# Kernel optimization log

Measured on AMD Instinct MI355X. Metric: run time of the kernel, lower is better.

Reference implementation:

```python
import jax, jax.numpy as jnp
import numpy as np

B, D_FEAT, D_ATTR, N_CLS = 512, 2048, 312, 150


def setup_inputs() -> dict:
    key = jax.random.key(0)
    k1, k2, k3, k4, k5 = jax.random.split(key, 5)
    return {
        "x_f": jax.random.normal(k1, (B, D_FEAT), dtype=jnp.float32),
        "W": jax.random.normal(k2, (D_FEAT, D_ATTR), dtype=jnp.float32) * 0.02,
        "b": jax.random.normal(k3, (D_ATTR,), dtype=jnp.float32) * 0.02,
        "seen_att": jax.random.normal(k4, (N_CLS, D_ATTR), dtype=jnp.float32),
        "x_labels": jax.random.randint(k5, (B,), 0, N_CLS, dtype=jnp.int64),
    }


def reference(x_f, W, b, seen_att, x_labels):
    temp = 1.0
    pre_attr = x_f @ W + b                                # [B, D]
    log_p = jax.nn.log_softmax(pre_attr / temp, axis=-1)  # log pre_attr_softmax
    log_g = jax.nn.log_softmax(seen_att[x_labels] / temp, axis=-1)
    g = jnp.exp(log_g)                                    # gt_attr_softmax [B, D]

    # pairwise KL(target = g_i/g_j || input_logits = log(p_i/p_j)), reduction='sum':
    #   sum_d t * (log t - log_ratio_p)
    t_ratio = g[:, None, :] / g[None, :, :]                               # [B, B, D]
    log_t = log_g[:, None, :] - log_g[None, :, :]                         # [B, B, D]
    log_r = log_p[:, None, :] - log_p[None, :, :]                         # [B, B, D]
    kl = jnp.sum(t_ratio * (log_t - log_r), axis=-1)                      # [B, B]

    same = x_labels[:, None] == x_labels[None, :]
    upper = jnp.triu(jnp.ones((x_labels.shape[0],) * 2, dtype=bool), k=1)
    mask = same & upper

    count = jnp.sum(mask)
    loss = jnp.sum(jnp.where(mask, kl, 0.0))
    return jnp.where(count > 0, loss / count.astype(loss.dtype), loss)
```

## Files before the change

### kernel.cpp

```cpp
#include <hip/hip_runtime.h>
#include <math.h>

#define B      512
#define DF     2048
#define DA     312
#define NTHR   320
#define RT     8
#define KSPLIT 16
#define NRG    (B / RT)

__device__ __forceinline__ float wave_max_f(float v) {
  #pragma unroll
  for (int off = 32; off >= 1; off >>= 1)
    v = fmaxf(v, __shfl_down(v, off));
  return v;
}

__device__ __forceinline__ double wave_sum_d(double v) {
  #pragma unroll
  for (int off = 32; off >= 1; off >>= 1)
    v += __shfl_down(v, off);
  return v;
}

template <int KC>
__global__ __launch_bounds__(NTHR, 5) void gemm_partial_kernel(
    const float* __restrict__ x_f, const float* __restrict__ W,
    float* __restrict__ part) {
  const int c    = threadIdx.x;
  const int rg   = blockIdx.x;
  const int ks   = blockIdx.y;
  const int row0 = rg * RT;
  const int k0   = ks * KC;
  const int ksplit = DF / KC;

  if (c >= DA) return;

  float acc[RT];
  #pragma unroll
  for (int r = 0; r < RT; ++r) acc[r] = 0.f;

  const float* Wp = W + (size_t)k0 * DA + c;
  const float* xp = x_f + (size_t)row0 * DF + k0;

  float wc[8];
  #pragma unroll
  for (int j = 0; j < 8; ++j) wc[j] = Wp[(size_t)j * DA];

  #pragma unroll
  for (int k = 0; k < KC; k += 8) {
    float wn[8];
    if (k + 8 < KC) {
      #pragma unroll
      for (int j = 0; j < 8; ++j) wn[j] = Wp[(size_t)(k + 8 + j) * DA];
    }
    #pragma unroll
    for (int r = 0; r < RT; ++r) {
      const float* xr = xp + (size_t)r * DF + k;
      #pragma unroll
      for (int j = 0; j < 8; ++j) acc[r] = fmaf(xr[j], wc[j], acc[r]);
    }
    if (k + 8 < KC) {
      #pragma unroll
      for (int j = 0; j < 8; ++j) wc[j] = wn[j];
    }
  }

  float* pp = part + ((size_t)(rg * ksplit + ks) * RT) * DA + c;
  #pragma unroll
  for (int r = 0; r < RT; ++r) pp[(size_t)r * DA] = acc[r];
}

template <int KS>
__global__ __launch_bounds__(NTHR) void row_stats_kernel(
    const float* __restrict__ part, const float* __restrict__ b,
    double* __restrict__ S) {
  __shared__ float  red_f[8];
  __shared__ double red_d[16];
  __shared__ float  bcast_max;

  const int tid  = threadIdx.x;
  const int wid  = tid >> 6;
  const int lane = tid & 63;
  const int row  = blockIdx.x;
  const int rg   = row / RT;
  const int r    = row & (RT - 1);

  float v = -INFINITY;
  if (tid < DA) {
    const float* pb = part + ((size_t)(rg * KS) * RT + r) * DA + tid;
    float ps[KS];
    #pragma unroll
    for (int p = 0; p < KS; ++p) ps[p] = pb[(size_t)p * RT * DA];
    float s = b[tid];
    #pragma unroll
    for (int p = 0; p < KS; ++p) s += ps[p];
    v = s;
  }

  float m = wave_max_f(v);
  if (lane == 0) red_f[wid] = m;
  __syncthreads();
  if (tid == 0) {
    float mm = red_f[0];
    #pragma unroll
    for (int w = 1; w < NTHR / 64; ++w) mm = fmaxf(mm, red_f[w]);
    bcast_max = mm;
  }
  __syncthreads();
  const float rowmax = bcast_max;

  double e  = (tid < DA) ? exp((double)v - (double)rowmax) : 0.0;
  double sp = (tid < DA) ? (double)v : 0.0;
  double es = wave_sum_d(e);
  double ss = wave_sum_d(sp);
  if (lane == 0) { red_d[wid] = es; red_d[8 + wid] = ss; }
  __syncthreads();
  if (tid == 0) {
    double esum = 0.0, ssum = 0.0;
    #pragma unroll
    for (int w = 0; w < NTHR / 64; ++w) { esum += red_d[w]; ssum += red_d[8 + w]; }
    S[row] = ssum - (double)DA * ((double)rowmax + log(esum));
  }
}

__global__ __launch_bounds__(1024) void pair_reduce_kernel(
    const double* __restrict__ S, const int* __restrict__ labels,
    float* __restrict__ out) {
  __shared__ double    Ss[B];
  __shared__ int       Ls[B];
  __shared__ double    red_d[16];
  __shared__ long long red_i[16];

  const int tid = threadIdx.x;
  if (tid < B) { Ss[tid] = S[tid]; Ls[tid] = labels[tid]; }
  __syncthreads();

  double lsum = 0.0;
  long long lcnt = 0;
  for (int p = tid; p < B * B; p += 1024) {
    int i = p >> 9;
    int j = p & (B - 1);
    if (j > i && Ls[i] == Ls[j]) { lsum += Ss[j] - Ss[i]; lcnt++; }
  }

  #pragma unroll
  for (int off = 32; off >= 1; off >>= 1) {
    lsum += __shfl_down(lsum, off);
    lcnt += __shfl_down(lcnt, off);
  }
  const int wid = tid >> 6, lane = tid & 63;
  if (lane == 0) { red_d[wid] = lsum; red_i[wid] = lcnt; }
  __syncthreads();
  if (tid == 0) {
    double s = 0.0; long long c = 0;
    #pragma unroll
    for (int w = 0; w < 16; ++w) { s += red_d[w]; c += red_i[w]; }
    out[0] = (float)((c > 0) ? s / (double)c : s);
  }
}

extern "C" void kernel_launch(void* const* d_in, const int* in_sizes, int n_in,
                              void* d_out, int out_size, void* d_ws, size_t ws_size,
                              hipStream_t stream) {
  const float* x_f    = (const float*)d_in[0];
  const float* W      = (const float*)d_in[1];
  const float* b      = (const float*)d_in[2];
  const int*   labels = (const int*)d_in[4];

  double* S    = (double*)d_ws;
  float*  part = (float*)((char*)d_ws + 4096);

  if (ws_size >= 4096 + (size_t)KSPLIT * B * DA * 4) {
    dim3 g1(NRG, KSPLIT);
    gemm_partial_kernel<DF / KSPLIT><<<g1, NTHR, 0, stream>>>(x_f, W, part);
    row_stats_kernel<KSPLIT><<<B, NTHR, 0, stream>>>(part, b, S);
  } else {
    dim3 g1(NRG, 2);
    gemm_partial_kernel<DF / 2><<<g1, NTHR, 0, stream>>>(x_f, W, part);
    row_stats_kernel<2><<<B, NTHR, 0, stream>>>(part, b, S);
  }
  pair_reduce_kernel<<<1, 1024, 0, stream>>>(S, labels, (float*)d_out);
}
```

Measured before the change: 112.7 us.

## Fuse split-K GEMM, row stats and pair reduction into one kernel with tickets

Replaces the three separate launches with a single kernel. The last split-K block to finish for each row group, found through an atomic ticket counter, reduces that group's partials and computes the row log-softmax sums. The last row group to finish then performs the pairwise masked reduction. This removes two kernel launches and their gaps, but adds a memset, atomic exchange stores, atomic loads that read through to the last-level cache, and a serial tail in which one 320-thread block does the B×B pair loop instead of a 1024-thread block.

```diff
diff --git a/kernel.cpp b/kernel.cpp
--- a/kernel.cpp
+++ b/kernel.cpp
@@ -8,6 +8,7 @@
 #define RT     8
 #define KSPLIT 16
 #define NRG    (B / RT)
+#define KC     (DF / KSPLIT)
 
 __device__ __forceinline__ float wave_max_f(float v) {
   #pragma unroll
@@ -23,49 +24,189 @@
   return v;
 }
 
-template <int KC>
-__global__ __launch_bounds__(NTHR, 5) void gemm_partial_kernel(
+__device__ __forceinline__ float llc_load_f(const float* p) {
+  return __int_as_float(atomicOr((int*)p, 0));
+}
+__device__ __forceinline__ double llc_load_d(const double* p) {
+  return __longlong_as_double(
+      (long long)atomicOr((unsigned long long*)p, 0ull));
+}
+
+__global__ __launch_bounds__(NTHR) void fused_kernel(
     const float* __restrict__ x_f, const float* __restrict__ W,
-    float* __restrict__ part) {
+    const float* __restrict__ b, const int* __restrict__ labels,
+    float* part, double* S, int* counters, float* out) {
   const int c    = threadIdx.x;
   const int rg   = blockIdx.x;
   const int ks   = blockIdx.y;
   const int row0 = rg * RT;
   const int k0   = ks * KC;
-  const int ksplit = DF / KC;
-
+
+  __shared__ int       ticket_sh;
+  __shared__ float     red_f[8];
+  __shared__ float     bcast_max;
+  __shared__ double    red_d[16];
+  __shared__ long long red_i[8];
+  __shared__ double    Ss[B];
+  __shared__ int       Ls[B];
+
+  if (c < DA) {
+    float acc[RT];
+    #pragma unroll
+    for (int r = 0; r < RT; ++r) acc[r] = 0.f;
+
+    const float* Wp = W + (size_t)k0 * DA + c;
+    const float* xp = x_f + (size_t)row0 * DF + k0;
+
+    float wc[8];
+    #pragma unroll
+    for (int j = 0; j < 8; ++j) wc[j] = Wp[(size_t)j * DA];
+
+    #pragma unroll
+    for (int k = 0; k < KC; k += 8) {
+      float wn[8];
+      if (k + 8 < KC) {
+        #pragma unroll
+        for (int j = 0; j < 8; ++j) wn[j] = Wp[(size_t)(k + 8 + j) * DA];
+      }
+      #pragma unroll
+      for (int r = 0; r < RT; ++r) {
+        const float* xr = xp + (size_t)r * DF + k;
+        #pragma unroll
+        for (int j = 0; j < 8; ++j) acc[r] = fmaf(xr[j], wc[j], acc[r]);
+      }
+      if (k + 8 < KC) {
+        #pragma unroll
+        for (int j = 0; j < 8; ++j) wc[j] = wn[j];
+      }
+    }
+
+    float* pp = part + ((size_t)(rg * KSPLIT + ks) * RT) * DA + c;
+    float sink = 0.f;
+    #pragma unroll
+    for (int r = 0; r < RT; ++r)
+      sink += atomicExch(&pp[(size_t)r * DA], acc[r]);
+    asm volatile("" :: "v"(sink));
+  }
+
+  asm volatile("s_waitcnt vmcnt(0)" ::: "memory");
+  __syncthreads();
+  if (threadIdx.x == 0)
+    ticket_sh = atomicAdd(&counters[rg], 1);
+  __syncthreads();
+  if (ticket_sh != KSPLIT - 1) return;
+
+  const int wid  = threadIdx.x >> 6;
+  const int lane = threadIdx.x & 63;
+
+  float s[RT];
+  if (c < DA) {
+    const float bias = b[c];
+    #pragma unroll
+    for (int r = 0; r < RT; ++r) {
+      float ps[KSPLIT];
+      #pragma unroll
+      for (int p = 0; p < KSPLIT; ++p)
+        ps[p] = llc_load_f(part + ((size_t)(rg * KSPLIT + p) * RT + r) * DA + c);
+      float acc2 = bias;
+      #pragma unroll
+      for (int p = 0; p < KSPLIT; ++p) acc2 += ps[p];
+      s[r] = acc2;
+    }
+  }
+
+  double ssink = 0.0;
+  for (int r = 0; r < RT; ++r) {
+    float v = (c < DA) ? s[r] : -INFINITY;
+    float m = wave_max_f(v);
+    if (lane == 0) red_f[wid] = m;
+    __syncthreads();
+    if (threadIdx.x == 0) {
+      float mm = red_f[0];
+      #pragma unroll
+      for (int w = 1; w < NTHR / 64; ++w) mm = fmaxf(mm, red_f[w]);
+      bcast_max = mm;
+    }
+    __syncthreads();
+    const float rowmax = bcast_max;
+
+    double e  = (c < DA) ? exp((double)v - (double)rowmax) : 0.0;
+    double sp = (c < DA) ? (double)v : 0.0;
+    double es = wave_sum_d(e);
+    double ss = wave_sum_d(sp);
+    if (lane == 0) { red_d[wid] = es; red_d[8 + wid] = ss; }
+    __syncthreads();
+    if (threadIdx.x == 0) {
+      double esum = 0.0, ssum = 0.0;
+      #pragma unroll
+      for (int w = 0; w < NTHR / 64; ++w) { esum += red_d[w]; ssum += red_d[8 + w]; }
+      double Sval = ssum - (double)DA * ((double)rowmax + log(esum));
+      ssink += __longlong_as_double((long long)atomicExch(
+          (unsigned long long*)&S[row0 + r],
+          (unsigned long long)__double_as_longlong(Sval)));
+    }
+    __syncthreads();
+  }
+  asm volatile("" :: "v"(ssink));
+
+  asm volatile("s_waitcnt vmcnt(0)" ::: "memory");
+  __syncthreads();
+  if (threadIdx.x == 0)
+    ticket_sh = atomicAdd(&counters[NRG], 1);
+  __syncthreads();
+  if (ticket_sh != NRG - 1) return;
+
+  for (int i = threadIdx.x; i < B; i += NTHR) {
+    Ss[i] = llc_load_d(&S[i]);
+    Ls[i] = labels[i];
+  }
+  __syncthreads();
+
+  double lsum = 0.0;
+  long long lcnt = 0;
+  for (int p = threadIdx.x; p < B * B; p += NTHR) {
+    int i = p >> 9;
+    int j = p & (B - 1);
+    if (j > i && Ls[i] == Ls[j]) { lsum += Ss[j] - Ss[i]; lcnt++; }
+  }
+  #pragma unroll
+  for (int off = 32; off >= 1; off >>= 1) {
+    lsum += __shfl_down(lsum, off);
+    lcnt += __shfl_down(lcnt, off);
+  }
+  if (lane == 0) { red_d[wid] = lsum; red_i[wid] = lcnt; }
+  __syncthreads();
+  if (threadIdx.x == 0) {
+    double s2 = 0.0; long long c2 = 0;
+    #pragma unroll
+    for (int w = 0; w < NTHR / 64; ++w) { s2 += red_d[w]; c2 += red_i[w]; }
+    out[0] = (float)((c2 > 0) ? s2 / (double)c2 : s2);
+  }
+}
+
+template <int KCF>
+__global__ __launch_bounds__(NTHR) void gemm_partial_kernel(
+    const float* __restrict__ x_f, const float* __restrict__ W,
+    float* __restrict__ part) {
+  const int c = threadIdx.x, rg = blockIdx.x, ks = blockIdx.y;
+  const int row0 = rg * RT, k0 = ks * KCF, ksplit = DF / KCF;
   if (c >= DA) return;
-
   float acc[RT];
   #pragma unroll
   for (int r = 0; r < RT; ++r) acc[r] = 0.f;
-
   const float* Wp = W + (size_t)k0 * DA + c;
   const float* xp = x_f + (size_t)row0 * DF + k0;
-
-  float wc[8];
-  #pragma unroll
-  for (int j = 0; j < 8; ++j) wc[j] = Wp[(size_t)j * DA];
-
-  #pragma unroll
-  for (int k = 0; k < KC; k += 8) {
-    float wn[8];
-    if (k + 8 < KC) {
-      #pragma unroll
-      for (int j = 0; j < 8; ++j) wn[j] = Wp[(size_t)(k + 8 + j) * DA];
-    }
+  for (int k = 0; k < KCF; k += 8) {
+    float w[8];
+    #pragma unroll
+    for (int j = 0; j < 8; ++j) w[j] = Wp[(size_t)(k + j) * DA];
     #pragma unroll
     for (int r = 0; r < RT; ++r) {
       const float* xr = xp + (size_t)r * DF + k;
       #pragma unroll
-      for (int j = 0; j < 8; ++j) acc[r] = fmaf(xr[j], wc[j], acc[r]);
-    }
-    if (k + 8 < KC) {
-      #pragma unroll
-      for (int j = 0; j < 8; ++j) wc[j] = wn[j];
-    }
-  }
-
+      for (int j = 0; j < 8; ++j) acc[r] = fmaf(xr[j], w[j], acc[r]);
+    }
+  }
   float* pp = part + ((size_t)(rg * ksplit + ks) * RT) * DA + c;
   #pragma unroll
   for (int r = 0; r < RT; ++r) pp[(size_t)r * DA] = acc[r];
@@ -78,26 +219,19 @@
   __shared__ float  red_f[8];
   __shared__ double red_d[16];
   __shared__ float  bcast_max;
-
-  const int tid  = threadIdx.x;
-  const int wid  = tid >> 6;
-  const int lane = tid & 63;
-  const int row  = blockIdx.x;
-  const int rg   = row / RT;
-  const int r    = row & (RT - 1);
-
+  const int tid = threadIdx.x, wid = tid >> 6, lane = tid & 63;
+  const int row = blockIdx.x, rg = row / RT, r = row & (RT - 1);
   float v = -INFINITY;
   if (tid < DA) {
     const float* pb = part + ((size_t)(rg * KS) * RT + r) * DA + tid;
     float ps[KS];
     #pragma unroll
     for (int p = 0; p < KS; ++p) ps[p] = pb[(size_t)p * RT * DA];
-    float s = b[tid];
-    #pragma unroll
-    for (int p = 0; p < KS; ++p) s += ps[p];
-    v = s;
-  }
-
+    float sv = b[tid];
+    #pragma unroll
+    for (int p = 0; p < KS; ++p) sv += ps[p];
+    v = sv;
+  }
   float m = wave_max_f(v);
   if (lane == 0) red_f[wid] = m;
   __syncthreads();
@@ -109,7 +243,6 @@
   }
   __syncthreads();
   const float rowmax = bcast_max;
-
   double e  = (tid < DA) ? exp((double)v - (double)rowmax) : 0.0;
   double sp = (tid < DA) ? (double)v : 0.0;
   double es = wave_sum_d(e);
@@ -131,19 +264,15 @@
   __shared__ int       Ls[B];
   __shared__ double    red_d[16];
   __shared__ long long red_i[16];
-
   const int tid = threadIdx.x;
   if (tid < B) { Ss[tid] = S[tid]; Ls[tid] = labels[tid]; }
   __syncthreads();
-
   double lsum = 0.0;
   long long lcnt = 0;
   for (int p = tid; p < B * B; p += 1024) {
-    int i = p >> 9;
-    int j = p & (B - 1);
+    int i = p >> 9, j = p & (B - 1);
     if (j > i && Ls[i] == Ls[j]) { lsum += Ss[j] - Ss[i]; lcnt++; }
   }
-
   #pragma unroll
   for (int off = 32; off >= 1; off >>= 1) {
     lsum += __shfl_down(lsum, off);
@@ -168,17 +297,21 @@
   const float* b      = (const float*)d_in[2];
   const int*   labels = (const int*)d_in[4];
 
-  double* S    = (double*)d_ws;
-  float*  part = (float*)((char*)d_ws + 4096);
-
-  if (ws_size >= 4096 + (size_t)KSPLIT * B * DA * 4) {
-    dim3 g1(NRG, KSPLIT);
-    gemm_partial_kernel<DF / KSPLIT><<<g1, NTHR, 0, stream>>>(x_f, W, part);
-    row_stats_kernel<KSPLIT><<<B, NTHR, 0, stream>>>(part, b, S);
+  const size_t need = 8192 + (size_t)KSPLIT * B * DA * 4;
+  if (ws_size >= need) {
+    int*    counters = (int*)d_ws;
+    double* S        = (double*)((char*)d_ws + 512);
+    float*  part     = (float*)((char*)d_ws + 8192);
+    hipMemsetAsync(d_ws, 0, 512, stream);
+    dim3 g(NRG, KSPLIT);
+    fused_kernel<<<g, NTHR, 0, stream>>>(x_f, W, b, labels, part, S, counters,
+                                         (float*)d_out);
   } else {
+    double* S    = (double*)d_ws;
+    float*  part = (float*)((char*)d_ws + 4096);
     dim3 g1(NRG, 2);
     gemm_partial_kernel<DF / 2><<<g1, NTHR, 0, stream>>>(x_f, W, part);
     row_stats_kernel<2><<<B, NTHR, 0, stream>>>(part, b, S);
-  }
-  pair_reduce_kernel<<<1, 1024, 0, stream>>>(S, labels, (float*)d_out);
-}
+    pair_reduce_kernel<<<1, 1024, 0, stream>>>(S, labels, (float*)d_out);
+  }
+}
```

Measured after the change: 196.0 us. +73.9%, slower.

## Fuse pair reduction into row-stats kernel via rank-weighted sum and last-block ticket

Applied to the files above, without the earlier changes.

Removes the separate single-block pair_reduce kernel, which scanned all B*B pairs serially on one workgroup. Each row block now computes its label rank and same-label count. It writes coef*S_i and its rank to global memory. A ticket atomic lets the last block finish the reduction, turning the O(B^2) pair loop into an O(B) weighted sum. The cost is an extra label scan per block, atomic/fence ordering that relies on relaxed atomics plus s_waitcnt, and one fewer kernel launch.

```diff
diff --git a/kernel.cpp b/kernel.cpp
--- a/kernel.cpp
+++ b/kernel.cpp
@@ -23,10 +23,23 @@
   return v;
 }
 
+__device__ __forceinline__ void dev_store_d(double* p, double v) {
+  __hip_atomic_store(p, v, __ATOMIC_RELAXED, __HIP_MEMORY_SCOPE_AGENT);
+}
+__device__ __forceinline__ double dev_load_d(const double* p) {
+  return __hip_atomic_load(p, __ATOMIC_RELAXED, __HIP_MEMORY_SCOPE_AGENT);
+}
+__device__ __forceinline__ void dev_store_i(int* p, int v) {
+  __hip_atomic_store(p, v, __ATOMIC_RELAXED, __HIP_MEMORY_SCOPE_AGENT);
+}
+__device__ __forceinline__ int dev_load_i(const int* p) {
+  return __hip_atomic_load(p, __ATOMIC_RELAXED, __HIP_MEMORY_SCOPE_AGENT);
+}
+
 template <int KC>
 __global__ __launch_bounds__(NTHR, 5) void gemm_partial_kernel(
     const float* __restrict__ x_f, const float* __restrict__ W,
-    float* __restrict__ part) {
+    float* __restrict__ part, int* ticket) {
   const int c    = threadIdx.x;
   const int rg   = blockIdx.x;
   const int ks   = blockIdx.y;
@@ -34,6 +47,9 @@
   const int k0   = ks * KC;
   const int ksplit = DF / KC;
 
+  if (blockIdx.x == 0 && blockIdx.y == 0 && threadIdx.x == 0)
+    *ticket = 0;
+
   if (c >= DA) return;
 
   float acc[RT];
@@ -72,12 +88,16 @@
 }
 
 template <int KS>
-__global__ __launch_bounds__(NTHR) void row_stats_kernel(
+__global__ __launch_bounds__(NTHR) void rowstats_pair_kernel(
     const float* __restrict__ part, const float* __restrict__ b,
-    double* __restrict__ S) {
+    const int* __restrict__ labels,
+    double* T, int* RK, int* ticket, float* __restrict__ out) {
   __shared__ float  red_f[8];
   __shared__ double red_d[16];
+  __shared__ int    red_i[16];
   __shared__ float  bcast_max;
+  __shared__ int    ticket_sh;
+  __shared__ int    Lsh[B];
 
   const int tid  = threadIdx.x;
   const int wid  = tid >> 6;
@@ -86,18 +106,150 @@
   const int rg   = row / RT;
   const int r    = row & (RT - 1);
 
+  for (int i = tid; i < B; i += NTHR) Lsh[i] = labels[i];
+
+  float v = -INFINITY;
+  float ps[KS];
+  const bool active = (tid < DA);
+  if (active) {
+    const float* pb = part + ((size_t)(rg * KS) * RT + r) * DA + tid;
+    #pragma unroll
+    for (int p = 0; p < KS; ++p) ps[p] = pb[(size_t)p * RT * DA];
+  }
+
+  __syncthreads();
+
+  const int myl = Lsh[row];
+  int c_less = 0, c_all = 0;
+  for (int j = tid; j < B; j += NTHR) {
+    const int same = (Lsh[j] == myl) ? 1 : 0;
+    c_all += same;
+    if (j < row) c_less += same;
+  }
+  #pragma unroll
+  for (int off = 32; off >= 1; off >>= 1) {
+    c_less += __shfl_down(c_less, off);
+    c_all  += __shfl_down(c_all,  off);
+  }
+  if (lane == 0) { red_i[wid] = c_less; red_i[8 + wid] = c_all; }
+
+  if (active) {
+    float s = b[tid];
+    #pragma unroll
+    for (int p = 0; p < KS; ++p) s += ps[p];
+    v = s;
+  }
+
+  float m = wave_max_f(v);
+  if (lane == 0) red_f[wid] = m;
+  __syncthreads();
+  if (tid == 0) {
+    float mm = red_f[0];
+    #pragma unroll
+    for (int w = 1; w < NTHR / 64; ++w) mm = fmaxf(mm, red_f[w]);
+    bcast_max = mm;
+  }
+  __syncthreads();
+  const float rowmax = bcast_max;
+
+  double e  = active ? exp((double)v - (double)rowmax) : 0.0;
+  double sp = active ? (double)v : 0.0;
+  double es = wave_sum_d(e);
+  double ss = wave_sum_d(sp);
+  if (lane == 0) { red_d[wid] = es; red_d[8 + wid] = ss; }
+  __syncthreads();
+  if (tid == 0) {
+    double esum = 0.0, ssum = 0.0;
+    int rank = 0, mcnt = 0;
+    #pragma unroll
+    for (int w = 0; w < NTHR / 64; ++w) {
+      esum += red_d[w]; ssum += red_d[8 + w];
+      rank += red_i[w]; mcnt += red_i[8 + w];
+    }
+    const double S    = ssum - (double)DA * ((double)rowmax + log(esum));
+    const double coef = (double)(2 * rank - mcnt + 1);
+    dev_store_d(&T[row], coef * S);
+    dev_store_i(&RK[row], rank);
+  }
+
+  asm volatile("s_waitcnt vmcnt(0)" ::: "memory");
+  __syncthreads();
+  if (tid == 0)
+    ticket_sh = __hip_atomic_fetch_add(ticket, 1, __ATOMIC_RELAXED,
+                                       __HIP_MEMORY_SCOPE_AGENT);
+  __syncthreads();
+  if (ticket_sh != B - 1) return;
+  asm volatile("" ::: "memory");
+
+  double tloc = 0.0;
+  int    rloc = 0;
+  for (int i = tid; i < B; i += NTHR) {
+    tloc += dev_load_d(&T[i]);
+    rloc += dev_load_i(&RK[i]);
+  }
+  #pragma unroll
+  for (int off = 32; off >= 1; off >>= 1) {
+    tloc += __shfl_down(tloc, off);
+    rloc += __shfl_down(rloc, off);
+  }
+  if (lane == 0) { red_d[wid] = tloc; red_i[wid] = rloc; }
+  __syncthreads();
+  if (tid == 0) {
+    double ts = 0.0; int rs = 0;
+    #pragma unroll
+    for (int w = 0; w < NTHR / 64; ++w) { ts += red_d[w]; rs += red_i[w]; }
+    out[0] = (float)((rs > 0) ? ts / (double)rs : ts);
+  }
+}
+
+template <int KCF>
+__global__ __launch_bounds__(NTHR) void gemm_partial_fb(
+    const float* __restrict__ x_f, const float* __restrict__ W,
+    float* __restrict__ part) {
+  const int c = threadIdx.x, rg = blockIdx.x, ks = blockIdx.y;
+  const int row0 = rg * RT, k0 = ks * KCF, ksplit = DF / KCF;
+  if (c >= DA) return;
+  float acc[RT];
+  #pragma unroll
+  for (int r = 0; r < RT; ++r) acc[r] = 0.f;
+  const float* Wp = W + (size_t)k0 * DA + c;
+  const float* xp = x_f + (size_t)row0 * DF + k0;
+  for (int k = 0; k < KCF; k += 8) {
+    float w[8];
+    #pragma unroll
+    for (int j = 0; j < 8; ++j) w[j] = Wp[(size_t)(k + j) * DA];
+    #pragma unroll
+    for (int r = 0; r < RT; ++r) {
+      const float* xr = xp + (size_t)r * DF + k;
+      #pragma unroll
+      for (int j = 0; j < 8; ++j) acc[r] = fmaf(xr[j], w[j], acc[r]);
+    }
+  }
+  float* pp = part + ((size_t)(rg * ksplit + ks) * RT) * DA + c;
+  #pragma unroll
+  for (int r = 0; r < RT; ++r) pp[(size_t)r * DA] = acc[r];
+}
+
+template <int KS>
+__global__ __launch_bounds__(NTHR) void row_stats_fb(
+    const float* __restrict__ part, const float* __restrict__ b,
+    double* __restrict__ S) {
+  __shared__ float  red_f[8];
+  __shared__ double red_d[16];
+  __shared__ float  bcast_max;
+  const int tid = threadIdx.x, wid = tid >> 6, lane = tid & 63;
+  const int row = blockIdx.x, rg = row / RT, r = row & (RT - 1);
   float v = -INFINITY;
   if (tid < DA) {
     const float* pb = part + ((size_t)(rg * KS) * RT + r) * DA + tid;
     float ps[KS];
     #pragma unroll
     for (int p = 0; p < KS; ++p) ps[p] = pb[(size_t)p * RT * DA];
-    float s = b[tid];
-    #pragma unroll
-    for (int p = 0; p < KS; ++p) s += ps[p];
-    v = s;
-  }
-
+    float sv = b[tid];
+    #pragma unroll
+    for (int p = 0; p < KS; ++p) sv += ps[p];
+    v = sv;
+  }
   float m = wave_max_f(v);
   if (lane == 0) red_f[wid] = m;
   __syncthreads();
@@ -109,7 +261,6 @@
   }
   __syncthreads();
   const float rowmax = bcast_max;
-
   double e  = (tid < DA) ? exp((double)v - (double)rowmax) : 0.0;
   double sp = (tid < DA) ? (double)v : 0.0;
   double es = wave_sum_d(e);
@@ -124,26 +275,22 @@
   }
 }
 
-__global__ __launch_bounds__(1024) void pair_reduce_kernel(
+__global__ __launch_bounds__(1024) void pair_reduce_fb(
     const double* __restrict__ S, const int* __restrict__ labels,
     float* __restrict__ out) {
   __shared__ double    Ss[B];
   __shared__ int       Ls[B];
   __shared__ double    red_d[16];
   __shared__ long long red_i[16];
-
   const int tid = threadIdx.x;
   if (tid < B) { Ss[tid] = S[tid]; Ls[tid] = labels[tid]; }
   __syncthreads();
-
   double lsum = 0.0;
   long long lcnt = 0;
   for (int p = tid; p < B * B; p += 1024) {
-    int i = p >> 9;
-    int j = p & (B - 1);
+    int i = p >> 9, j = p & (B - 1);
     if (j > i && Ls[i] == Ls[j]) { lsum += Ss[j] - Ss[i]; lcnt++; }
   }
-
   #pragma unroll
   for (int off = 32; off >= 1; off >>= 1) {
     lsum += __shfl_down(lsum, off);
@@ -168,17 +315,23 @@
   const float* b      = (const float*)d_in[2];
   const int*   labels = (const int*)d_in[4];
 
-  double* S    = (double*)d_ws;
-  float*  part = (float*)((char*)d_ws + 4096);
-
-  if (ws_size >= 4096 + (size_t)KSPLIT * B * DA * 4) {
+  const size_t need = 16384 + (size_t)KSPLIT * B * DA * 4;
+  if (ws_size >= need) {
+    int*    ticket = (int*)d_ws;
+    double* T      = (double*)((char*)d_ws + 4096);
+    int*    RK     = (int*)((char*)d_ws + 8192);
+    float*  part   = (float*)((char*)d_ws + 16384);
     dim3 g1(NRG, KSPLIT);
-    gemm_partial_kernel<DF / KSPLIT><<<g1, NTHR, 0, stream>>>(x_f, W, part);
-    row_stats_kernel<KSPLIT><<<B, NTHR, 0, stream>>>(part, b, S);
+    gemm_partial_kernel<DF / KSPLIT><<<g1, NTHR, 0, stream>>>(x_f, W, part,
+                                                              ticket);
+    rowstats_pair_kernel<KSPLIT><<<B, NTHR, 0, stream>>>(
+        part, b, labels, T, RK, ticket, (float*)d_out);
   } else {
+    double* S    = (double*)d_ws;
+    float*  part = (float*)((char*)d_ws + 4096);
     dim3 g1(NRG, 2);
-    gemm_partial_kernel<DF / 2><<<g1, NTHR, 0, stream>>>(x_f, W, part);
-    row_stats_kernel<2><<<B, NTHR, 0, stream>>>(part, b, S);
-  }
-  pair_reduce_kernel<<<1, 1024, 0, stream>>>(S, labels, (float*)d_out);
-}
+    gemm_partial_fb<DF / 2><<<g1, NTHR, 0, stream>>>(x_f, W, part);
+    row_stats_fb<2><<<B, NTHR, 0, stream>>>(part, b, S);
+    pair_reduce_fb<<<1, 1024, 0, stream>>>(S, labels, (float*)d_out);
+  }
+}
```

Result: faster. 93.94 us (-16.6%).
